# Kernel tuning notes

Hardware: AMD Instinct MI355X
Metric: run time of the kernel (lower is better)

The kernel has to match this reference:

```python
import jax, jax.numpy as jnp
import numpy as np

CUTOFF = 5.0
N_RBF = 20

A = 50000
F = 128
E = 500000


def setup_inputs() -> dict:
    key = jax.random.key(0)
    ks = jax.random.split(key, 10)
    return {
        "vectors": jax.random.normal(ks[0], (A, 3, F), dtype=jnp.float32),
        "scalars": jax.random.normal(ks[1], (A, 1, F), dtype=jnp.float32),
        "directions": jax.random.normal(ks[2], (E, 3), dtype=jnp.float32),
        "idx_i": jax.random.randint(ks[3], (E,), 0, A),
        "idx_j": jax.random.randint(ks[4], (E,), 0, A),
        "W1": jax.random.normal(ks[5], (F, F), dtype=jnp.float32) / np.sqrt(F),
        "b1": jnp.zeros((F,), dtype=jnp.float32),
        "W2": jax.random.normal(ks[6], (F, 3 * F), dtype=jnp.float32) / np.sqrt(F),
        "b2": jnp.zeros((3 * F,), dtype=jnp.float32),
        "Wr": jax.random.normal(ks[7], (N_RBF, 3 * F), dtype=jnp.float32) / np.sqrt(N_RBF),
        "br": jnp.zeros((3 * F,), dtype=jnp.float32),
    }


def reference(vectors, scalars, directions, idx_i, idx_j, W1, b1, W2, b2, Wr, br):
    feat = scalars.shape[-1]
    n_nodes = vectors.shape[0]
    n_rbf = Wr.shape[0]

    s = jax.nn.silu(scalars @ W1 + b1) @ W2 + b2

    # edge norms: E x 1
    norm_r = jnp.sqrt(jnp.sum(directions * directions, axis=-1, keepdims=True))

    # radial basis: sin(k*pi/rc * |r|)/|r|  -> E x n
    rr = jnp.arange(1, n_rbf + 1, dtype=directions.dtype)
    rbf = jnp.sin(rr * (jnp.pi / CUTOFF) * norm_r) / norm_r
    r = rbf @ Wr + br  # E x 3F

    # cosine cutoff with hard mask (min(delta,0)/delta == 1 inside cutoff, 0 outside)
    delta = norm_r - CUTOFF
    mask = jnp.minimum(delta, 0.0) / delta
    fc = 0.5 * (jnp.cos(jnp.pi * norm_r / CUTOFF) + 1.0) * mask
    r = fc * r  # E x 3F

    combined = s[idx_i] * r[:, None, :]
    delta_s, delta_v1, delta_v2 = jnp.split(combined, 3, axis=-1)

    delta_v = vectors[idx_i] * delta_v1 + delta_v2 * (directions / norm_r)[:, :, None]

    # scatter-add back to nodes
    delta_s = jax.ops.segment_sum(delta_s, idx_j, num_segments=n_nodes)
    delta_v = jax.ops.segment_sum(delta_v, idx_j, num_segments=n_nodes)
    return delta_v, delta_s
```

## Files before the change

### kernel.cpp

```cpp
#include <hip/hip_runtime.h>
#include <math.h>

#define A_NODES 50000
#define FEAT 128
#define EDGES 500000
#define NRBF 20
#define CUTOFF_F 5.0f
#define PI_OVER_CUTOFF 0.6283185307179586f

typedef unsigned int uint32;
typedef unsigned short ushort16;
typedef short bf16x8 __attribute__((ext_vector_type(8)));
typedef float f32x4 __attribute__((ext_vector_type(4)));
typedef float f32x2 __attribute__((ext_vector_type(2)));

__device__ __forceinline__ ushort16 f2bf(float f) {
    union { float f; uint32 u; } v; v.f = f;
    uint32 r = (v.u + 0x7fffu + ((v.u >> 16) & 1u)) >> 16;
    return (ushort16)r;
}
__device__ __forceinline__ uint32 packbf(float a, float b) {
    return (uint32)f2bf(a) | ((uint32)f2bf(b) << 16);
}
__device__ __forceinline__ float bf_lo(uint32 u) { return __uint_as_float(u << 16); }
__device__ __forceinline__ float bf_hi(uint32 u) { return __uint_as_float(u & 0xffff0000u); }

#if __has_builtin(__builtin_amdgcn_fdot2_f32_bf16)
typedef __bf16 bf16x2 __attribute__((ext_vector_type(2)));
__device__ __forceinline__ float dot2(uint32 a, uint32 b, float c) {
    return __builtin_amdgcn_fdot2_f32_bf16(
        __builtin_bit_cast(bf16x2, a), __builtin_bit_cast(bf16x2, b), c, false);
}
#else
__device__ __forceinline__ float dot2(uint32 a, uint32 b, float c) {
    return fmaf(bf_hi(a), bf_hi(b), fmaf(bf_lo(a), bf_lo(b), c));
}
#endif

__global__ __launch_bounds__(256) void pack_kernel(
    const float* __restrict__ W1, const float* __restrict__ W2,
    const float* __restrict__ Wr,
    ushort16* __restrict__ w1pk, ushort16* __restrict__ w2pk,
    uint32* __restrict__ wrpk)
{
    const int t = blockIdx.x * 256 + threadIdx.x;
    if (t < 16384) {
        const int jj = t & 7, l = (t >> 3) & 63, kk = (t >> 9) & 3, nt = t >> 11;
        const int col = (l & 15) + 16 * nt;
        const int k   = kk * 32 + (l >> 4) * 8 + jj;
        w1pk[t] = f2bf(W1[k * 128 + col]);
    } else if (t < 16384 + 49152) {
        const int u = t - 16384;
        const int jj = u & 7, l = (u >> 3) & 63, kk = (u >> 9) & 3, nt = u >> 11;
        const int col = (l & 15) + 16 * nt;
        const int k   = kk * 32 + (l >> 4) * 8 + jj;
        w2pk[u] = f2bf(W2[k * 384 + col]);
    } else if (t < 16384 + 49152 + 3840) {
        const int u = t - 16384 - 49152;
        const int m = u / 384, col = u % 384;
        wrpk[u] = packbf(Wr[(2 * m) * 384 + col], Wr[(2 * m + 1) * 384 + col]);
    }
}

__global__ __launch_bounds__(256) void node_mlp_kernel(
    const float* __restrict__ scalars,
    const ushort16* __restrict__ w1pk, const float* __restrict__ bias1,
    const ushort16* __restrict__ w2pk, const float* __restrict__ bias2,
    ushort16* __restrict__ s_bf)
{
    __shared__ ushort16 sc[16][136];
    __shared__ ushort16 hd[16][136];
    const int tx   = threadIdx.x;
    const int lane = tx & 63;
    const int wv   = tx >> 6;
    const int base = blockIdx.x * 16;

    {
        const int row = tx >> 4;
        const int cs  = (tx & 15) * 8;
        const float* src = scalars + (size_t)(base + row) * FEAT + cs;
        const float4 f0 = *(const float4*)src;
        const float4 f1 = *(const float4*)(src + 4);
        bf16x8 tmp;
        tmp[0] = (short)f2bf(f0.x); tmp[1] = (short)f2bf(f0.y);
        tmp[2] = (short)f2bf(f0.z); tmp[3] = (short)f2bf(f0.w);
        tmp[4] = (short)f2bf(f1.x); tmp[5] = (short)f2bf(f1.y);
        tmp[6] = (short)f2bf(f1.z); tmp[7] = (short)f2bf(f1.w);
        *(bf16x8*)&sc[row][cs] = tmp;
    }
    __syncthreads();

    const int arow = lane & 15;
    const int kgrp = lane >> 4;

    f32x4 acc0 = {0.f, 0.f, 0.f, 0.f};
    f32x4 acc1 = {0.f, 0.f, 0.f, 0.f};
    #pragma unroll
    for (int kk = 0; kk < 4; ++kk) {
        const bf16x8 a  = *(const bf16x8*)&sc[arow][kk * 32 + kgrp * 8];
        const bf16x8 b0 = *(const bf16x8*)(w1pk + (((size_t)(wv * 2 + 0) * 4 + kk) * 64 + lane) * 8);
        const bf16x8 b1 = *(const bf16x8*)(w1pk + (((size_t)(wv * 2 + 1) * 4 + kk) * 64 + lane) * 8);
        acc0 = __builtin_amdgcn_mfma_f32_16x16x32_bf16(a, b0, acc0, 0, 0, 0);
        acc1 = __builtin_amdgcn_mfma_f32_16x16x32_bf16(a, b1, acc1, 0, 0, 0);
    }
    {
        const int c0 = wv * 32 + (lane & 15);
        const int c1 = c0 + 16;
        const float bb0 = bias1[c0], bb1 = bias1[c1];
        #pragma unroll
        for (int r = 0; r < 4; ++r) {
            const int row = kgrp * 4 + r;
            float x0 = acc0[r] + bb0;
            float x1 = acc1[r] + bb1;
            x0 = x0 / (1.0f + __expf(-x0));
            x1 = x1 / (1.0f + __expf(-x1));
            hd[row][c0] = f2bf(x0);
            hd[row][c1] = f2bf(x1);
        }
    }
    __syncthreads();

    f32x4 acc[6];
    #pragma unroll
    for (int n = 0; n < 6; ++n) acc[n] = (f32x4){0.f, 0.f, 0.f, 0.f};
    #pragma unroll
    for (int kk = 0; kk < 4; ++kk) {
        const bf16x8 a = *(const bf16x8*)&hd[arow][kk * 32 + kgrp * 8];
        #pragma unroll
        for (int n = 0; n < 6; ++n) {
            const bf16x8 b = *(const bf16x8*)(w2pk + (((size_t)(wv * 6 + n) * 4 + kk) * 64 + lane) * 8);
            acc[n] = __builtin_amdgcn_mfma_f32_16x16x32_bf16(a, b, acc[n], 0, 0, 0);
        }
    }
    #pragma unroll
    for (int n = 0; n < 6; ++n) {
        const int col = (wv * 6 + n) * 16 + (lane & 15);
        const float bb = bias2[col];
        #pragma unroll
        for (int r = 0; r < 4; ++r) {
            const int row = kgrp * 4 + r;
            s_bf[(size_t)(base + row) * 384 + col] = f2bf(acc[n][r] + bb);
        }
    }
}

__global__ __launch_bounds__(256) void vec_cvt_kernel(
    const float* __restrict__ vin, uint4* __restrict__ vbf)
{
    const size_t t = (size_t)blockIdx.x * 256 + threadIdx.x;
    const size_t n8 = (size_t)A_NODES * 384 / 8;
    if (t < n8) {
        const float4 f0 = ((const float4*)vin)[2 * t];
        const float4 f1 = ((const float4*)vin)[2 * t + 1];
        uint4 o;
        o.x = packbf(f0.x, f0.y); o.y = packbf(f0.z, f0.w);
        o.z = packbf(f1.x, f1.y); o.w = packbf(f1.z, f1.w);
        vbf[t] = o;
    }
}

__global__ __launch_bounds__(256) void hist_kernel(
    const int* __restrict__ idx_j, int* __restrict__ hist)
{
    const int e = blockIdx.x * 256 + threadIdx.x;
    if (e < EDGES) atomicAdd(&hist[idx_j[e]], 1);
}

__global__ __launch_bounds__(1024) void scan_kernel(
    const int* __restrict__ hist, int* __restrict__ offsets,
    int* __restrict__ cursor)
{
    __shared__ int part[1024];
    const int t = threadIdx.x;
    const int CH = (A_NODES + 1023) / 1024;

    int sum = 0;
    for (int k = 0; k < CH; ++k) {
        const int idx = t * CH + k;
        if (idx < A_NODES) sum += hist[idx];
    }
    part[t] = sum;
    __syncthreads();
    for (int off = 1; off < 1024; off <<= 1) {
        const int v = (t >= off) ? part[t - off] : 0;
        __syncthreads();
        part[t] += v;
        __syncthreads();
    }
    int run = part[t] - sum;
    for (int k = 0; k < CH; ++k) {
        const int idx = t * CH + k;
        if (idx < A_NODES) {
            offsets[idx] = run;
            cursor[idx]  = run;
            run += hist[idx];
        }
    }
    if (t == 0) offsets[A_NODES] = EDGES;
}

__global__ __launch_bounds__(256) void edge_prep_kernel(
    const float* __restrict__ directions,
    const int* __restrict__ idx_i, const int* __restrict__ idx_j,
    int* __restrict__ cursor,
    float* __restrict__ edata)
{
    const int e = blockIdx.x * 256 + threadIdx.x;
    if (e >= EDGES) return;
    const int j   = idx_j[e];
    const int pos = atomicAdd(&cursor[j], 1);
    const int i   = idx_i[e];
    const float d0 = directions[(size_t)e * 3 + 0];
    const float d1 = directions[(size_t)e * 3 + 1];
    const float d2 = directions[(size_t)e * 3 + 2];
    const float nr   = sqrtf(d0 * d0 + d1 * d1 + d2 * d2);
    const float invn = 1.0f / nr;
    const float x = PI_OVER_CUTOFF * nr;
    float sx, cx;
    sincosf(x, &sx, &cx);
    const float fc = (nr < CUTOFF_F) ? 0.5f * (cx + 1.0f) : 0.0f;
    const float scale = invn * fc;
    const float twoc = 2.0f * cx;

    float out16[16];
    float s_odd = sx;
    float s_prev = 0.0f;
    #pragma unroll
    for (int m = 0; m < 10; ++m) {
        const float s_even = twoc * s_odd - s_prev;
        out16[m] = __uint_as_float(packbf(s_odd * scale, s_even * scale));
        const float s_next = twoc * s_even - s_odd;
        s_prev = s_even;
        s_odd  = s_next;
    }
    out16[10] = d0 * invn;
    out16[11] = d1 * invn;
    out16[12] = d2 * invn;
    out16[13] = fc;
    out16[14] = __int_as_float(i);
    out16[15] = 0.0f;

    float4* dst = (float4*)(edata + (size_t)pos * 16);
    dst[0] = make_float4(out16[0],  out16[1],  out16[2],  out16[3]);
    dst[1] = make_float4(out16[4],  out16[5],  out16[6],  out16[7]);
    dst[2] = make_float4(out16[8],  out16[9],  out16[10], out16[11]);
    dst[3] = make_float4(out16[12], out16[13], out16[14], out16[15]);
}

template <int VBF>
__global__ __launch_bounds__(256, 4) void gather_kernel(
    const ushort16* __restrict__ s_bf,
    const ushort16* __restrict__ v_bf,
    const float* __restrict__ vectors_f32,
    const uint32* __restrict__ wrpk, const float* __restrict__ br,
    const float* __restrict__ edata,
    const int* __restrict__ offsets,
    float* __restrict__ out_v, float* __restrict__ out_s)
{
    const int lane = threadIdx.x & 63;
    const int wv   = threadIdx.x >> 6;
    const int j    = blockIdx.x * 4 + wv;
    const int c0   = lane * 2;

#define LDW(s, m) (*(const uint2*)(wrpk + (m) * 384 + (s) * 128 + c0))
    const uint2 w00 = LDW(0,0), w01 = LDW(0,1), w02 = LDW(0,2), w03 = LDW(0,3), w04 = LDW(0,4);
    const uint2 w05 = LDW(0,5), w06 = LDW(0,6), w07 = LDW(0,7), w08 = LDW(0,8), w09 = LDW(0,9);
    const uint2 w10 = LDW(1,0), w11 = LDW(1,1), w12 = LDW(1,2), w13 = LDW(1,3), w14 = LDW(1,4);
    const uint2 w15 = LDW(1,5), w16 = LDW(1,6), w17 = LDW(1,7), w18 = LDW(1,8), w19 = LDW(1,9);
    const uint2 w20 = LDW(2,0), w21 = LDW(2,1), w22 = LDW(2,2), w23 = LDW(2,3), w24 = LDW(2,4);
    const uint2 w25 = LDW(2,5), w26 = LDW(2,6), w27 = LDW(2,7), w28 = LDW(2,8), w29 = LDW(2,9);
#undef LDW
    const float2 brv0 = *(const float2*)(br + c0);
    const float2 brv1 = *(const float2*)(br + 128 + c0);
    const float2 brv2 = *(const float2*)(br + 256 + c0);

    const int beg = offsets[j];
    const int end = offsets[j + 1];

    float accsA = 0.f, accsB = 0.f;
    float avA0 = 0.f, avA1 = 0.f, avA2 = 0.f;
    float avB0 = 0.f, avB1 = 0.f, avB2 = 0.f;

    int p = beg;
    float4 cA, cB, cC, cD;
    if (p < end) {
        const float4* s0p = (const float4*)(edata + (size_t)p * 16);
        cA = s0p[0]; cB = s0p[1]; cC = s0p[2]; cD = s0p[3];
    }

    while (p < end) {
        const int pn = p + 1;
        const int i  = __float_as_int(cD.z);

        const ushort16* srow = s_bf + (size_t)i * 384;
        const uint32 s0 = *(const uint32*)(srow + c0);
        const uint32 s1 = *(const uint32*)(srow + 128 + c0);
        const uint32 s2 = *(const uint32*)(srow + 256 + c0);

        float vA0, vB0, vA1, vB1, vA2, vB2;
        if (VBF) {
            const ushort16* vrow = v_bf + (size_t)i * 384;
            const uint32 v0 = *(const uint32*)(vrow + c0);
            const uint32 v1 = *(const uint32*)(vrow + 128 + c0);
            const uint32 v2 = *(const uint32*)(vrow + 256 + c0);
            vA0 = bf_lo(v0); vB0 = bf_hi(v0);
            vA1 = bf_lo(v1); vB1 = bf_hi(v1);
            vA2 = bf_lo(v2); vB2 = bf_hi(v2);
        } else {
            const float* vrow = vectors_f32 + (size_t)i * 384;
            vA0 = vrow[c0];       vB0 = vrow[c0 + 1];
            vA1 = vrow[128 + c0]; vB1 = vrow[129 + c0];
            vA2 = vrow[256 + c0]; vB2 = vrow[257 + c0];
        }

        const size_t pf = (size_t)(pn < end ? pn : p) * 16;
        const float4* sn = (const float4*)(edata + pf);
        const float4 nA = sn[0], nB = sn[1], nC = sn[2], nD = sn[3];

        const uint32 b0 = __float_as_uint(cA.x), b1 = __float_as_uint(cA.y);
        const uint32 b2 = __float_as_uint(cA.z), b3 = __float_as_uint(cA.w);
        const uint32 b4 = __float_as_uint(cB.x), b5 = __float_as_uint(cB.y);
        const uint32 b6 = __float_as_uint(cB.z), b7 = __float_as_uint(cB.w);
        const uint32 b8 = __float_as_uint(cC.x), b9 = __float_as_uint(cC.y);
        const float u0 = cC.z, u1 = cC.w, u2 = cD.x, fcv = cD.y;

        float rA0 = fcv * brv0.x, rB0 = fcv * brv0.y;
        float rA1 = fcv * brv1.x, rB1 = fcv * brv1.y;
        float rA2 = fcv * brv2.x, rB2 = fcv * brv2.y;

#define DOTS(bb, wa, wb, wc) \
        rA0 = dot2(bb, wa.x, rA0); rB0 = dot2(bb, wa.y, rB0); \
        rA1 = dot2(bb, wb.x, rA1); rB1 = dot2(bb, wb.y, rB1); \
        rA2 = dot2(bb, wc.x, rA2); rB2 = dot2(bb, wc.y, rB2);
        DOTS(b0, w00, w10, w20)
        DOTS(b1, w01, w11, w21)
        DOTS(b2, w02, w12, w22)
        DOTS(b3, w03, w13, w23)
        DOTS(b4, w04, w14, w24)
        DOTS(b5, w05, w15, w25)
        DOTS(b6, w06, w16, w26)
        DOTS(b7, w07, w17, w27)
        DOTS(b8, w08, w18, w28)
        DOTS(b9, w09, w19, w29)
#undef DOTS

        const float sA0 = bf_lo(s0), sB0 = bf_hi(s0);
        const float sA1 = bf_lo(s1), sB1 = bf_hi(s1);
        const float sA2 = bf_lo(s2), sB2 = bf_hi(s2);

        accsA = fmaf(sA0, rA0, accsA);
        accsB = fmaf(sB0, rB0, accsB);
        const float gA1 = sA1 * rA1, gA2 = sA2 * rA2;
        const float gB1 = sB1 * rB1, gB2 = sB2 * rB2;

        avA0 = fmaf(vA0, gA1, fmaf(gA2, u0, avA0));
        avB0 = fmaf(vB0, gB1, fmaf(gB2, u0, avB0));
        avA1 = fmaf(vA1, gA1, fmaf(gA2, u1, avA1));
        avB1 = fmaf(vB1, gB1, fmaf(gB2, u1, avB1));
        avA2 = fmaf(vA2, gA1, fmaf(gA2, u2, avA2));
        avB2 = fmaf(vB2, gB1, fmaf(gB2, u2, avB2));

        cA = nA; cB = nB; cC = nC; cD = nD;
        p = pn;
    }

    f32x2 t;
    t.x = accsA; t.y = accsB;
    __builtin_nontemporal_store(t, (f32x2*)(out_s + (size_t)j * 128 + c0));
    float* ov = out_v + (size_t)j * 384;
    t.x = avA0; t.y = avB0;
    __builtin_nontemporal_store(t, (f32x2*)(ov + c0));
    t.x = avA1; t.y = avB1;
    __builtin_nontemporal_store(t, (f32x2*)(ov + 128 + c0));
    t.x = avA2; t.y = avB2;
    __builtin_nontemporal_store(t, (f32x2*)(ov + 256 + c0));
}

extern "C" void kernel_launch(void* const* d_in, const int* in_sizes, int n_in,
                              void* d_out, int out_size, void* d_ws, size_t ws_size,
                              hipStream_t stream) {
    const float* vectors    = (const float*)d_in[0];
    const float* scalars    = (const float*)d_in[1];
    const float* directions = (const float*)d_in[2];
    const int*   idx_i      = (const int*)d_in[3];
    const int*   idx_j      = (const int*)d_in[4];
    const float* W1         = (const float*)d_in[5];
    const float* b1         = (const float*)d_in[6];
    const float* W2         = (const float*)d_in[7];
    const float* b2         = (const float*)d_in[8];
    const float* Wr         = (const float*)d_in[9];
    const float* br         = (const float*)d_in[10];

    float* out_v = (float*)d_out;
    float* out_s = out_v + (size_t)A_NODES * 3 * FEAT;

    char* ws = (char*)d_ws;
    ushort16* s_bf = (ushort16*)ws;  ws += (size_t)A_NODES * 384 * 2;
    float* edata   = (float*)ws;     ws += (size_t)EDGES * 16 * 4;
    uint32* wrpk   = (uint32*)ws;    ws += (size_t)10 * 384 * 4;
    ushort16* w1pk = (ushort16*)ws;  ws += (size_t)16384 * 2;
    ushort16* w2pk = (ushort16*)ws;  ws += (size_t)49152 * 2;
    int* hist      = (int*)ws;       ws += (size_t)A_NODES * 4;
    int* offsets   = (int*)ws;       ws += (((size_t)(A_NODES + 1) * 4 + 15) & ~(size_t)15);
    int* cursor    = (int*)ws;       ws += (size_t)A_NODES * 4;
    ushort16* v_bf = (ushort16*)ws;  ws += (size_t)A_NODES * 384 * 2;

    const int use_vbf = ((size_t)(ws - (char*)d_ws) <= ws_size) ? 1 : 0;

    hipMemsetAsync(hist, 0, (size_t)A_NODES * 4, stream);

    pack_kernel<<<271, 256, 0, stream>>>(W1, W2, Wr, w1pk, w2pk, wrpk);
    node_mlp_kernel<<<A_NODES / 16, 256, 0, stream>>>(scalars, w1pk, b1, w2pk, b2, s_bf);
    if (use_vbf)
        vec_cvt_kernel<<<(int)(((size_t)A_NODES * 384 / 8 + 255) / 256), 256, 0, stream>>>(
            vectors, (uint4*)v_bf);

    hist_kernel<<<(EDGES + 255) / 256, 256, 0, stream>>>(idx_j, hist);
    scan_kernel<<<1, 1024, 0, stream>>>(hist, offsets, cursor);
    edge_prep_kernel<<<(EDGES + 255) / 256, 256, 0, stream>>>(
        directions, idx_i, idx_j, cursor, edata);

    if (use_vbf)
        gather_kernel<1><<<A_NODES / 4, 256, 0, stream>>>(
            s_bf, v_bf, vectors, wrpk, br, edata, offsets, out_v, out_s);
    else
        gather_kernel<0><<<A_NODES / 4, 256, 0, stream>>>(
            s_bf, v_bf, vectors, wrpk, br, edata, offsets, out_v, out_s);
}
```

Baseline: 571.6 us.

## Split each node's edges across two waves, stage Wr in LDS, merge prep kernels

The gather kernel now gives each destination node two wavefronts. Each wave processes two edges per iteration with strided interleaving, and the partial sums are combined through shared memory. The Wr weights move from per-thread registers into LDS, which lowers register pressure and frees room for two edges in flight per wave. The vector conversion, histogram and weight packing kernels are merged into one launch to cut launch overhead. The costs are an added block-wide sync, an LDS reduction, and twice as many blocks.

```diff
diff --git a/kernel.cpp b/kernel.cpp
--- a/kernel.cpp
+++ b/kernel.cpp
@@ -37,28 +37,52 @@
 }
 #endif
 
-__global__ __launch_bounds__(256) void pack_kernel(
+#define NB_CVT 9375
+#define NB_HIST 1954
+#define NB_PACK 271
+
+__global__ __launch_bounds__(256) void prep_kernel(
+    const float* __restrict__ vin, uint4* __restrict__ vbf, int use_vbf,
+    const int* __restrict__ idx_j, int* __restrict__ hist,
     const float* __restrict__ W1, const float* __restrict__ W2,
     const float* __restrict__ Wr,
     ushort16* __restrict__ w1pk, ushort16* __restrict__ w2pk,
     uint32* __restrict__ wrpk)
 {
-    const int t = blockIdx.x * 256 + threadIdx.x;
-    if (t < 16384) {
-        const int jj = t & 7, l = (t >> 3) & 63, kk = (t >> 9) & 3, nt = t >> 11;
-        const int col = (l & 15) + 16 * nt;
-        const int k   = kk * 32 + (l >> 4) * 8 + jj;
-        w1pk[t] = f2bf(W1[k * 128 + col]);
-    } else if (t < 16384 + 49152) {
-        const int u = t - 16384;
-        const int jj = u & 7, l = (u >> 3) & 63, kk = (u >> 9) & 3, nt = u >> 11;
-        const int col = (l & 15) + 16 * nt;
-        const int k   = kk * 32 + (l >> 4) * 8 + jj;
-        w2pk[u] = f2bf(W2[k * 384 + col]);
-    } else if (t < 16384 + 49152 + 3840) {
-        const int u = t - 16384 - 49152;
-        const int m = u / 384, col = u % 384;
-        wrpk[u] = packbf(Wr[(2 * m) * 384 + col], Wr[(2 * m + 1) * 384 + col]);
+    const int b = blockIdx.x;
+    if (b < NB_CVT) {
+        if (!use_vbf) return;
+        const size_t t = (size_t)b * 256 + threadIdx.x;
+        const size_t n8 = (size_t)A_NODES * 384 / 8;
+        if (t < n8) {
+            const float4 f0 = ((const float4*)vin)[2 * t];
+            const float4 f1 = ((const float4*)vin)[2 * t + 1];
+            uint4 o;
+            o.x = packbf(f0.x, f0.y); o.y = packbf(f0.z, f0.w);
+            o.z = packbf(f1.x, f1.y); o.w = packbf(f1.z, f1.w);
+            vbf[t] = o;
+        }
+    } else if (b < NB_CVT + NB_HIST) {
+        const int e = (b - NB_CVT) * 256 + threadIdx.x;
+        if (e < EDGES) atomicAdd(&hist[idx_j[e]], 1);
+    } else {
+        const int t = (b - NB_CVT - NB_HIST) * 256 + threadIdx.x;
+        if (t < 16384) {
+            const int jj = t & 7, l = (t >> 3) & 63, kk = (t >> 9) & 3, nt = t >> 11;
+            const int col = (l & 15) + 16 * nt;
+            const int k   = kk * 32 + (l >> 4) * 8 + jj;
+            w1pk[t] = f2bf(W1[k * 128 + col]);
+        } else if (t < 16384 + 49152) {
+            const int u = t - 16384;
+            const int jj = u & 7, l = (u >> 3) & 63, kk = (u >> 9) & 3, nt = u >> 11;
+            const int col = (l & 15) + 16 * nt;
+            const int k   = kk * 32 + (l >> 4) * 8 + jj;
+            w2pk[u] = f2bf(W2[k * 384 + col]);
+        } else if (t < 16384 + 49152 + 3840) {
+            const int u = t - 16384 - 49152;
+            const int m = u / 384, col = u % 384;
+            wrpk[u] = packbf(Wr[(2 * m) * 384 + col], Wr[(2 * m + 1) * 384 + col]);
+        }
     }
 }
 
@@ -142,28 +166,6 @@
             s_bf[(size_t)(base + row) * 384 + col] = f2bf(acc[n][r] + bb);
         }
     }
-}
-
-__global__ __launch_bounds__(256) void vec_cvt_kernel(
-    const float* __restrict__ vin, uint4* __restrict__ vbf)
-{
-    const size_t t = (size_t)blockIdx.x * 256 + threadIdx.x;
-    const size_t n8 = (size_t)A_NODES * 384 / 8;
-    if (t < n8) {
-        const float4 f0 = ((const float4*)vin)[2 * t];
-        const float4 f1 = ((const float4*)vin)[2 * t + 1];
-        uint4 o;
-        o.x = packbf(f0.x, f0.y); o.y = packbf(f0.z, f0.w);
-        o.z = packbf(f1.x, f1.y); o.w = packbf(f1.z, f1.w);
-        vbf[t] = o;
-    }
-}
-
-__global__ __launch_bounds__(256) void hist_kernel(
-    const int* __restrict__ idx_j, int* __restrict__ hist)
-{
-    const int e = blockIdx.x * 256 + threadIdx.x;
-    if (e < EDGES) atomicAdd(&hist[idx_j[e]], 1);
 }
 
 __global__ __launch_bounds__(1024) void scan_kernel(
@@ -240,11 +242,11 @@
     out16[14] = __int_as_float(i);
     out16[15] = 0.0f;
 
-    float4* dst = (float4*)(edata + (size_t)pos * 16);
-    dst[0] = make_float4(out16[0],  out16[1],  out16[2],  out16[3]);
-    dst[1] = make_float4(out16[4],  out16[5],  out16[6],  out16[7]);
-    dst[2] = make_float4(out16[8],  out16[9],  out16[10], out16[11]);
-    dst[3] = make_float4(out16[12], out16[13], out16[14], out16[15]);
+    f32x4* dst = (f32x4*)(edata + (size_t)pos * 16);
+    dst[0] = (f32x4){out16[0],  out16[1],  out16[2],  out16[3]};
+    dst[1] = (f32x4){out16[4],  out16[5],  out16[6],  out16[7]};
+    dst[2] = (f32x4){out16[8],  out16[9],  out16[10], out16[11]};
+    dst[3] = (f32x4){out16[12], out16[13], out16[14], out16[15]};
 }
 
 template <int VBF>
@@ -257,19 +259,22 @@
     const int* __restrict__ offsets,
     float* __restrict__ out_v, float* __restrict__ out_s)
 {
-    const int lane = threadIdx.x & 63;
-    const int wv   = threadIdx.x >> 6;
-    const int j    = blockIdx.x * 4 + wv;
+    __shared__ uint32 lds_w[3840];
+    __shared__ float red[4][64][9];
+
+    const int tx   = threadIdx.x;
+    const int lane = tx & 63;
+    const int wv   = __builtin_amdgcn_readfirstlane(tx >> 6);
+    const int nsub = wv >> 1;
+    const int par  = wv & 1;
+    const int j    = blockIdx.x * 2 + nsub;
     const int c0   = lane * 2;
 
-#define LDW(s, m) (*(const uint2*)(wrpk + (m) * 384 + (s) * 128 + c0))
-    const uint2 w00 = LDW(0,0), w01 = LDW(0,1), w02 = LDW(0,2), w03 = LDW(0,3), w04 = LDW(0,4);
-    const uint2 w05 = LDW(0,5), w06 = LDW(0,6), w07 = LDW(0,7), w08 = LDW(0,8), w09 = LDW(0,9);
-    const uint2 w10 = LDW(1,0), w11 = LDW(1,1), w12 = LDW(1,2), w13 = LDW(1,3), w14 = LDW(1,4);
-    const uint2 w15 = LDW(1,5), w16 = LDW(1,6), w17 = LDW(1,7), w18 = LDW(1,8), w19 = LDW(1,9);
-    const uint2 w20 = LDW(2,0), w21 = LDW(2,1), w22 = LDW(2,2), w23 = LDW(2,3), w24 = LDW(2,4);
-    const uint2 w25 = LDW(2,5), w26 = LDW(2,6), w27 = LDW(2,7), w28 = LDW(2,8), w29 = LDW(2,9);
-#undef LDW
+    #pragma unroll
+    for (int q = 0; q < 15; ++q)
+        lds_w[tx + q * 256] = wrpk[tx + q * 256];
+    __syncthreads();
+
     const float2 brv0 = *(const float2*)(br + c0);
     const float2 brv1 = *(const float2*)(br + 128 + c0);
     const float2 brv2 = *(const float2*)(br + 256 + c0);
@@ -281,99 +286,149 @@
     float avA0 = 0.f, avA1 = 0.f, avA2 = 0.f;
     float avB0 = 0.f, avB1 = 0.f, avB2 = 0.f;
 
-    int p = beg;
-    float4 cA, cB, cC, cD;
-    if (p < end) {
-        const float4* s0p = (const float4*)(edata + (size_t)p * 16);
-        cA = s0p[0]; cB = s0p[1]; cC = s0p[2]; cD = s0p[3];
-    }
-
-    while (p < end) {
-        const int pn = p + 1;
-        const int i  = __float_as_int(cD.z);
-
-        const ushort16* srow = s_bf + (size_t)i * 384;
-        const uint32 s0 = *(const uint32*)(srow + c0);
-        const uint32 s1 = *(const uint32*)(srow + 128 + c0);
-        const uint32 s2 = *(const uint32*)(srow + 256 + c0);
-
-        float vA0, vB0, vA1, vB1, vA2, vB2;
+    for (int p = beg + 2 * par; p < end; p += 4) {
+        const int p1 = p + 1;
+        const int ok1 = (p1 < end);
+        const int p1c = ok1 ? p1 : p;
+
+        const f32x4* q0p = (const f32x4*)(edata + (size_t)p * 16);
+        const f32x4 a0 = q0p[0], a1 = q0p[1], a2 = q0p[2], a3 = q0p[3];
+        const f32x4* q1p = (const f32x4*)(edata + (size_t)p1c * 16);
+        const f32x4 b0q = q1p[0], b1q = q1p[1], b2q = q1p[2], b3q = q1p[3];
+
+        const int i0 = __float_as_int(a3.z);
+        const int i1 = __float_as_int(b3q.z);
+
+        const ushort16* sr0 = s_bf + (size_t)i0 * 384;
+        const uint32 s00 = *(const uint32*)(sr0 + c0);
+        const uint32 s01 = *(const uint32*)(sr0 + 128 + c0);
+        const uint32 s02 = *(const uint32*)(sr0 + 256 + c0);
+        const ushort16* sr1 = s_bf + (size_t)i1 * 384;
+        const uint32 s10 = *(const uint32*)(sr1 + c0);
+        const uint32 s11 = *(const uint32*)(sr1 + 128 + c0);
+        const uint32 s12 = *(const uint32*)(sr1 + 256 + c0);
+
+        float v0A0, v0B0, v0A1, v0B1, v0A2, v0B2;
+        float v1A0, v1B0, v1A1, v1B1, v1A2, v1B2;
         if (VBF) {
-            const ushort16* vrow = v_bf + (size_t)i * 384;
-            const uint32 v0 = *(const uint32*)(vrow + c0);
-            const uint32 v1 = *(const uint32*)(vrow + 128 + c0);
-            const uint32 v2 = *(const uint32*)(vrow + 256 + c0);
-            vA0 = bf_lo(v0); vB0 = bf_hi(v0);
-            vA1 = bf_lo(v1); vB1 = bf_hi(v1);
-            vA2 = bf_lo(v2); vB2 = bf_hi(v2);
+            const ushort16* vr0 = v_bf + (size_t)i0 * 384;
+            const uint32 x0 = *(const uint32*)(vr0 + c0);
+            const uint32 x1 = *(const uint32*)(vr0 + 128 + c0);
+            const uint32 x2 = *(const uint32*)(vr0 + 256 + c0);
+            const ushort16* vr1 = v_bf + (size_t)i1 * 384;
+            const uint32 y0 = *(const uint32*)(vr1 + c0);
+            const uint32 y1 = *(const uint32*)(vr1 + 128 + c0);
+            const uint32 y2 = *(const uint32*)(vr1 + 256 + c0);
+            v0A0 = bf_lo(x0); v0B0 = bf_hi(x0);
+            v0A1 = bf_lo(x1); v0B1 = bf_hi(x1);
+            v0A2 = bf_lo(x2); v0B2 = bf_hi(x2);
+            v1A0 = bf_lo(y0); v1B0 = bf_hi(y0);
+            v1A1 = bf_lo(y1); v1B1 = bf_hi(y1);
+            v1A2 = bf_lo(y2); v1B2 = bf_hi(y2);
         } else {
-            const float* vrow = vectors_f32 + (size_t)i * 384;
-            vA0 = vrow[c0];       vB0 = vrow[c0 + 1];
-            vA1 = vrow[128 + c0]; vB1 = vrow[129 + c0];
-            vA2 = vrow[256 + c0]; vB2 = vrow[257 + c0];
-        }
-
-        const size_t pf = (size_t)(pn < end ? pn : p) * 16;
-        const float4* sn = (const float4*)(edata + pf);
-        const float4 nA = sn[0], nB = sn[1], nC = sn[2], nD = sn[3];
-
-        const uint32 b0 = __float_as_uint(cA.x), b1 = __float_as_uint(cA.y);
-        const uint32 b2 = __float_as_uint(cA.z), b3 = __float_as_uint(cA.w);
-        const uint32 b4 = __float_as_uint(cB.x), b5 = __float_as_uint(cB.y);
-        const uint32 b6 = __float_as_uint(cB.z), b7 = __float_as_uint(cB.w);
-        const uint32 b8 = __float_as_uint(cC.x), b9 = __float_as_uint(cC.y);
-        const float u0 = cC.z, u1 = cC.w, u2 = cD.x, fcv = cD.y;
-
-        float rA0 = fcv * brv0.x, rB0 = fcv * brv0.y;
-        float rA1 = fcv * brv1.x, rB1 = fcv * brv1.y;
-        float rA2 = fcv * brv2.x, rB2 = fcv * brv2.y;
-
-#define DOTS(bb, wa, wb, wc) \
-        rA0 = dot2(bb, wa.x, rA0); rB0 = dot2(bb, wa.y, rB0); \
-        rA1 = dot2(bb, wb.x, rA1); rB1 = dot2(bb, wb.y, rB1); \
-        rA2 = dot2(bb, wc.x, rA2); rB2 = dot2(bb, wc.y, rB2);
-        DOTS(b0, w00, w10, w20)
-        DOTS(b1, w01, w11, w21)
-        DOTS(b2, w02, w12, w22)
-        DOTS(b3, w03, w13, w23)
-        DOTS(b4, w04, w14, w24)
-        DOTS(b5, w05, w15, w25)
-        DOTS(b6, w06, w16, w26)
-        DOTS(b7, w07, w17, w27)
-        DOTS(b8, w08, w18, w28)
-        DOTS(b9, w09, w19, w29)
-#undef DOTS
-
-        const float sA0 = bf_lo(s0), sB0 = bf_hi(s0);
-        const float sA1 = bf_lo(s1), sB1 = bf_hi(s1);
-        const float sA2 = bf_lo(s2), sB2 = bf_hi(s2);
-
-        accsA = fmaf(sA0, rA0, accsA);
-        accsB = fmaf(sB0, rB0, accsB);
-        const float gA1 = sA1 * rA1, gA2 = sA2 * rA2;
-        const float gB1 = sB1 * rB1, gB2 = sB2 * rB2;
-
-        avA0 = fmaf(vA0, gA1, fmaf(gA2, u0, avA0));
-        avB0 = fmaf(vB0, gB1, fmaf(gB2, u0, avB0));
-        avA1 = fmaf(vA1, gA1, fmaf(gA2, u1, avA1));
-        avB1 = fmaf(vB1, gB1, fmaf(gB2, u1, avB1));
-        avA2 = fmaf(vA2, gA1, fmaf(gA2, u2, avA2));
-        avB2 = fmaf(vB2, gB1, fmaf(gB2, u2, avB2));
-
-        cA = nA; cB = nB; cC = nC; cD = nD;
-        p = pn;
-    }
-
-    f32x2 t;
-    t.x = accsA; t.y = accsB;
-    __builtin_nontemporal_store(t, (f32x2*)(out_s + (size_t)j * 128 + c0));
-    float* ov = out_v + (size_t)j * 384;
-    t.x = avA0; t.y = avB0;
-    __builtin_nontemporal_store(t, (f32x2*)(ov + c0));
-    t.x = avA1; t.y = avB1;
-    __builtin_nontemporal_store(t, (f32x2*)(ov + 128 + c0));
-    t.x = avA2; t.y = avB2;
-    __builtin_nontemporal_store(t, (f32x2*)(ov + 256 + c0));
+            const float* vr0 = vectors_f32 + (size_t)i0 * 384;
+            v0A0 = vr0[c0];       v0B0 = vr0[c0 + 1];
+            v0A1 = vr0[128 + c0]; v0B1 = vr0[129 + c0];
+            v0A2 = vr0[256 + c0]; v0B2 = vr0[257 + c0];
+            const float* vr1 = vectors_f32 + (size_t)i1 * 384;
+            v1A0 = vr1[c0];       v1B0 = vr1[c0 + 1];
+            v1A1 = vr1[128 + c0]; v1B1 = vr1[129 + c0];
+            v1A2 = vr1[256 + c0]; v1B2 = vr1[257 + c0];
+        }
+
+        const uint32 e0m0 = __float_as_uint(a0.x), e0m1 = __float_as_uint(a0.y);
+        const uint32 e0m2 = __float_as_uint(a0.z), e0m3 = __float_as_uint(a0.w);
+        const uint32 e0m4 = __float_as_uint(a1.x), e0m5 = __float_as_uint(a1.y);
+        const uint32 e0m6 = __float_as_uint(a1.z), e0m7 = __float_as_uint(a1.w);
+        const uint32 e0m8 = __float_as_uint(a2.x), e0m9 = __float_as_uint(a2.y);
+        const uint32 e1m0 = __float_as_uint(b0q.x), e1m1 = __float_as_uint(b0q.y);
+        const uint32 e1m2 = __float_as_uint(b0q.z), e1m3 = __float_as_uint(b0q.w);
+        const uint32 e1m4 = __float_as_uint(b1q.x), e1m5 = __float_as_uint(b1q.y);
+        const uint32 e1m6 = __float_as_uint(b1q.z), e1m7 = __float_as_uint(b1q.w);
+        const uint32 e1m8 = __float_as_uint(b2q.x), e1m9 = __float_as_uint(b2q.y);
+
+        const float u00 = a2.z, u01 = a2.w, u02 = a3.x, fc0 = a3.y;
+        const float u10 = b2q.z, u11 = b2q.w, u12 = b3q.x, fc1 = b3q.y;
+
+        float r0A0 = fc0 * brv0.x, r0B0 = fc0 * brv0.y;
+        float r0A1 = fc0 * brv1.x, r0B1 = fc0 * brv1.y;
+        float r0A2 = fc0 * brv2.x, r0B2 = fc0 * brv2.y;
+        float r1A0 = fc1 * brv0.x, r1B0 = fc1 * brv0.y;
+        float r1A1 = fc1 * brv1.x, r1B1 = fc1 * brv1.y;
+        float r1A2 = fc1 * brv2.x, r1B2 = fc1 * brv2.y;
+
+#define WSTEP(M, R0, R1) { \
+        const uint2 wa = *(const uint2*)&lds_w[(M) * 384 + c0]; \
+        const uint2 wb = *(const uint2*)&lds_w[(M) * 384 + 128 + c0]; \
+        const uint2 wc = *(const uint2*)&lds_w[(M) * 384 + 256 + c0]; \
+        r0A0 = dot2(R0, wa.x, r0A0); r0B0 = dot2(R0, wa.y, r0B0); \
+        r0A1 = dot2(R0, wb.x, r0A1); r0B1 = dot2(R0, wb.y, r0B1); \
+        r0A2 = dot2(R0, wc.x, r0A2); r0B2 = dot2(R0, wc.y, r0B2); \
+        r1A0 = dot2(R1, wa.x, r1A0); r1B0 = dot2(R1, wa.y, r1B0); \
+        r1A1 = dot2(R1, wb.x, r1A1); r1B1 = dot2(R1, wb.y, r1B1); \
+        r1A2 = dot2(R1, wc.x, r1A2); r1B2 = dot2(R1, wc.y, r1B2); }
+        WSTEP(0, e0m0, e1m0)
+        WSTEP(1, e0m1, e1m1)
+        WSTEP(2, e0m2, e1m2)
+        WSTEP(3, e0m3, e1m3)
+        WSTEP(4, e0m4, e1m4)
+        WSTEP(5, e0m5, e1m5)
+        WSTEP(6, e0m6, e1m6)
+        WSTEP(7, e0m7, e1m7)
+        WSTEP(8, e0m8, e1m8)
+        WSTEP(9, e0m9, e1m9)
+#undef WSTEP
+
+        {
+            const float gA1 = bf_lo(s01) * r0A1, gA2 = bf_lo(s02) * r0A2;
+            const float gB1 = bf_hi(s01) * r0B1, gB2 = bf_hi(s02) * r0B2;
+            accsA = fmaf(bf_lo(s00), r0A0, accsA);
+            accsB = fmaf(bf_hi(s00), r0B0, accsB);
+            avA0 = fmaf(v0A0, gA1, fmaf(gA2, u00, avA0));
+            avB0 = fmaf(v0B0, gB1, fmaf(gB2, u00, avB0));
+            avA1 = fmaf(v0A1, gA1, fmaf(gA2, u01, avA1));
+            avB1 = fmaf(v0B1, gB1, fmaf(gB2, u01, avB1));
+            avA2 = fmaf(v0A2, gA1, fmaf(gA2, u02, avA2));
+            avB2 = fmaf(v0B2, gB1, fmaf(gB2, u02, avB2));
+        }
+        {
+            float t0A = bf_lo(s10) * r1A0, t0B = bf_hi(s10) * r1B0;
+            float gA1 = bf_lo(s11) * r1A1, gA2 = bf_lo(s12) * r1A2;
+            float gB1 = bf_hi(s11) * r1B1, gB2 = bf_hi(s12) * r1B2;
+            t0A = ok1 ? t0A : 0.f;  t0B = ok1 ? t0B : 0.f;
+            gA1 = ok1 ? gA1 : 0.f;  gA2 = ok1 ? gA2 : 0.f;
+            gB1 = ok1 ? gB1 : 0.f;  gB2 = ok1 ? gB2 : 0.f;
+            accsA += t0A;
+            accsB += t0B;
+            avA0 = fmaf(v1A0, gA1, fmaf(gA2, u10, avA0));
+            avB0 = fmaf(v1B0, gB1, fmaf(gB2, u10, avB0));
+            avA1 = fmaf(v1A1, gA1, fmaf(gA2, u11, avA1));
+            avB1 = fmaf(v1B1, gB1, fmaf(gB2, u11, avB1));
+            avA2 = fmaf(v1A2, gA1, fmaf(gA2, u12, avA2));
+            avB2 = fmaf(v1B2, gB1, fmaf(gB2, u12, avB2));
+        }
+    }
+
+    float* slot = red[wv][lane];
+    slot[0] = accsA; slot[1] = accsB;
+    slot[2] = avA0;  slot[3] = avB0;
+    slot[4] = avA1;  slot[5] = avB1;
+    slot[6] = avA2;  slot[7] = avB2;
+    __syncthreads();
+
+    if (par == 0) {
+        const float* o = red[wv | 1][lane];
+        f32x2 t;
+        t.x = accsA + o[0]; t.y = accsB + o[1];
+        __builtin_nontemporal_store(t, (f32x2*)(out_s + (size_t)j * 128 + c0));
+        float* ov = out_v + (size_t)j * 384;
+        t.x = avA0 + o[2]; t.y = avB0 + o[3];
+        __builtin_nontemporal_store(t, (f32x2*)(ov + c0));
+        t.x = avA1 + o[4]; t.y = avB1 + o[5];
+        __builtin_nontemporal_store(t, (f32x2*)(ov + 128 + c0));
+        t.x = avA2 + o[6]; t.y = avB2 + o[7];
+        __builtin_nontemporal_store(t, (f32x2*)(ov + 256 + c0));
+    }
 }
 
 extern "C" void kernel_launch(void* const* d_in, const int* in_sizes, int n_in,
@@ -409,21 +464,19 @@
 
     hipMemsetAsync(hist, 0, (size_t)A_NODES * 4, stream);
 
-    pack_kernel<<<271, 256, 0, stream>>>(W1, W2, Wr, w1pk, w2pk, wrpk);
+    prep_kernel<<<NB_CVT + NB_HIST + NB_PACK, 256, 0, stream>>>(
+        vectors, (uint4*)v_bf, use_vbf, idx_j, hist,
+        W1, W2, Wr, w1pk, w2pk, wrpk);
+
     node_mlp_kernel<<<A_NODES / 16, 256, 0, stream>>>(scalars, w1pk, b1, w2pk, b2, s_bf);
-    if (use_vbf)
-        vec_cvt_kernel<<<(int)(((size_t)A_NODES * 384 / 8 + 255) / 256), 256, 0, stream>>>(
-            vectors, (uint4*)v_bf);
-
-    hist_kernel<<<(EDGES + 255) / 256, 256, 0, stream>>>(idx_j, hist);
     scan_kernel<<<1, 1024, 0, stream>>>(hist, offsets, cursor);
     edge_prep_kernel<<<(EDGES + 255) / 256, 256, 0, stream>>>(
         directions, idx_i, idx_j, cursor, edata);
 
     if (use_vbf)
-        gather_kernel<1><<<A_NODES / 4, 256, 0, stream>>>(
+        gather_kernel<1><<<A_NODES / 2, 256, 0, stream>>>(
             s_bf, v_bf, vectors, wrpk, br, edata, offsets, out_v, out_s);
     else
-        gather_kernel<0><<<A_NODES / 4, 256, 0, stream>>>(
+        gather_kernel<0><<<A_NODES / 2, 256, 0, stream>>>(
             s_bf, v_bf, vectors, wrpk, br, edata, offsets, out_v, out_s);
 }
```

Result: faster. 523.9 us (-8.3%).
